# Optimization experiments

Hardware: AMD Instinct MI355X
Metric: run time of the kernel (lower is better)

Reference implementation:

```python
import jax, jax.numpy as jnp
import numpy as np

EPS = 1e-5
NEG = -1000000000.0

def _layernorm(x, g, b):
    m = x.mean(-1, keepdims=True)
    v = ((x - m) ** 2).mean(-1, keepdims=True)
    return (x - m) / jnp.sqrt(v + EPS) * g + b

D_MODEL, N_HEADS, D_K, D_V, D_FF = 768, 12, 64, 64, 3072
VOCAB, MAX_POS, N_LAYERS = 32000, 2048, 2
B, S = 2, 2048

def setup_inputs() -> dict:
    key = jax.random.key(0)
    ks = jax.random.split(key, 16)
    sc = 0.02
    L = N_LAYERS
    return {
        "inputs": jax.random.randint(ks[0], (B, S), 0, VOCAB, dtype=jnp.int64) if jax.config.jax_enable_x64 else jax.random.randint(ks[0], (B, S), 0, VOCAB, dtype=jnp.int32),
        "attention_mask": jax.random.randint(ks[1], (B, S), 0, 2, dtype=jnp.int32),
        "emb": jax.random.normal(ks[2], (VOCAB, D_MODEL), jnp.float32) * sc,
        "pos_emb": jax.random.normal(ks[3], (MAX_POS, D_MODEL), jnp.float32) * sc,
        "wq": jax.random.normal(ks[4], (L, D_MODEL, N_HEADS * D_K), jnp.float32) * sc,
        "wk": jax.random.normal(ks[5], (L, D_MODEL, N_HEADS * D_K), jnp.float32) * sc,
        "wv": jax.random.normal(ks[6], (L, D_MODEL, N_HEADS * D_V), jnp.float32) * sc,
        "wo": jax.random.normal(ks[7], (L, N_HEADS * D_V, D_MODEL), jnp.float32) * sc,
        "ln1_g": jnp.ones((L, D_MODEL), jnp.float32),
        "ln1_b": jnp.zeros((L, D_MODEL), jnp.float32),
        "w1": jax.random.normal(ks[8], (L, D_MODEL, D_FF), jnp.float32) * sc,
        "b1": jnp.zeros((L, D_FF), jnp.float32),
        "w2": jax.random.normal(ks[9], (L, D_FF, D_MODEL), jnp.float32) * sc,
        "b2": jnp.zeros((L, D_MODEL), jnp.float32),
        "ln2_g": jnp.ones((L, D_MODEL), jnp.float32),
        "ln2_b": jnp.zeros((L, D_MODEL), jnp.float32),
    }

def reference(inputs, attention_mask, emb, pos_emb, wq, wk, wv, wo,
              ln1_g, ln1_b, w1, b1, w2, b2, ln2_g, ln2_b):
    b, s = inputs.shape
    x = emb[inputs] + pos_emb[jnp.arange(s)][None, :, :]  # [B,S,D]
    # combined mask: True where pad token OR strictly-upper (future) position
    sub = jnp.triu(jnp.ones((s, s), dtype=bool), k=1)            # [S,S]
    pad = (attention_mask == 0)[:, None, :]                      # [B,1,S]
    mask = (pad | sub[None, :, :])[:, None, :, :]                # [B,1,S,S] -> broadcast over heads
    # FAITHFUL to source: masked_fill(attention_mask == 0, -1e9) fills where mask is FALSE
    scale = 1.0 / float(np.sqrt(D_K))
    attns = []
    for l in range(N_LAYERS):
        q = (x @ wq[l]).reshape(b, s, N_HEADS, D_K).transpose(0, 2, 1, 3)  # [B,H,S,dk]
        k = (x @ wk[l]).reshape(b, s, N_HEADS, D_K).transpose(0, 2, 1, 3)
        v = (x @ wv[l]).reshape(b, s, N_HEADS, D_V).transpose(0, 2, 1, 3)
        scores = jnp.einsum('bhqd,bhkd->bhqk', q, k) * scale
        scores = jnp.where(mask, scores, NEG)  # fill -1e9 where mask == False (as in source)
        attn = jax.nn.softmax(scores, axis=-1)
        ctx = jnp.einsum('bhqk,bhkd->bhqd', attn, v)
        ctx = ctx.transpose(0, 2, 1, 3).reshape(b, s, N_HEADS * D_V)
        x = _layernorm(ctx @ wo[l] + x, ln1_g[l], ln1_b[l])
        ff = jnp.maximum(x @ w1[l] + b1[l], 0.0) @ w2[l] + b2[l]
        x = _layernorm(ff + x, ln2_g[l], ln2_b[l])
        attns.append(attn)
    return x, jnp.stack(attns)  # [B,S,D], [L,B,H,S,S]
```

## Files before the change

### kernel.cpp

```cpp
#include <hip/hip_runtime.h>
#include <math.h>

#define DM 768
#define NH 12
#define DK 64
#define DFF 3072
#define BB 2
#define SS 2048
#define NL 2

typedef __attribute__((ext_vector_type(8))) short short8;
typedef __attribute__((ext_vector_type(4))) float f32x4;
typedef __attribute__((ext_vector_type(2))) unsigned int u32x2;

__device__ inline unsigned short f2bf(float f) {
    unsigned int u = __float_as_uint(f);
    u += 0x7fffu + ((u >> 16) & 1u);
    return (unsigned short)(u >> 16);
}
__device__ inline float bf2f(unsigned short h) {
    return __uint_as_float(((unsigned int)h) << 16);
}

#define GL16(g, l) __builtin_amdgcn_global_load_lds( \
    (const __attribute__((address_space(1))) void*)(g), \
    (__attribute__((address_space(3))) void*)(l), 16, 0, 0)

__global__ __launch_bounds__(256) void embed_kernel(
    const int* __restrict__ toks, const float* __restrict__ emb,
    const float* __restrict__ pos, float* __restrict__ x,
    unsigned short* __restrict__ xb)
{
    int rs = blockIdx.x;
    int s = rs & (SS - 1);
    int tok = toks[rs];
    int t = threadIdx.x;
    const float* e = emb + (size_t)tok * DM;
    const float* p = pos + (size_t)s * DM;
    float* xr = x + (size_t)rs * DM;
    unsigned short* xbr = xb + (size_t)rs * DM;
#pragma unroll
    for (int i = 0; i < 3; ++i) {
        int c = t + 256 * i;
        float v = e[c] + p[c];
        xr[c] = v;
        xbr[c] = f2bf(v);
    }
}

__global__ __launch_bounds__(256) void prep_weights(
    const float* __restrict__ wq, const float* __restrict__ wk,
    const float* __restrict__ wv, const float* __restrict__ wo,
    const float* __restrict__ w1, const float* __restrict__ w2,
    unsigned short* __restrict__ wt)
{
    __shared__ float tile[32][33];
    int id = blockIdx.x;
    int l = id / 6912; id -= l * 6912;
    unsigned short* wtl = wt + (size_t)l * 7077888;
    const float* src; unsigned short* dst; int Kd, Nd, nt, kt;
    if (id < 2304) {
        int m = id / 576, r = id % 576;
        src = ((m == 0) ? wq : (m == 1) ? wk : (m == 2) ? wv : wo) + (size_t)l * DM * DM;
        dst = wtl + (size_t)m * 589824;
        Kd = 768; Nd = 768; nt = r / 24; kt = r % 24;
    } else if (id < 4608) {
        int r = id - 2304;
        src = w1 + (size_t)l * DM * DFF; dst = wtl + 2359296; Kd = 768; Nd = 3072;
        nt = r / 24; kt = r % 24;
    } else {
        int r = id - 4608;
        src = w2 + (size_t)l * DFF * DM; dst = wtl + 4718592; Kd = 3072; Nd = 768;
        nt = r / 96; kt = r % 96;
    }
    int n0 = nt * 32, k0 = kt * 32;
    int c = threadIdx.x & 31, rr = threadIdx.x >> 5;
#pragma unroll
    for (int i = 0; i < 32; i += 8)
        tile[rr + i][c] = src[(size_t)(k0 + rr + i) * Nd + n0 + c];
    __syncthreads();
#pragma unroll
    for (int i = 0; i < 32; i += 8)
        dst[(size_t)(n0 + rr + i) * Kd + k0 + c] = f2bf(tile[c][rr + i]);
}

__global__ __launch_bounds__(256) void transpose_v(
    const unsigned short* __restrict__ vb, unsigned short* __restrict__ vt)
{
    __shared__ unsigned short tile[32][33];
    int c0 = blockIdx.x * 32;
    int r0 = blockIdx.y * 32;
    int c = threadIdx.x & 31, rr = threadIdx.x >> 5;
#pragma unroll
    for (int i = 0; i < 32; i += 8)
        tile[rr + i][c] = vb[(size_t)(r0 + rr + i) * DM + c0 + c];
    __syncthreads();
    int b = r0 >> 11;
    int s0 = r0 & 2047;
#pragma unroll
    for (int i = 0; i < 32; i += 8)
        vt[((size_t)b * DM + c0 + rr + i) * SS + s0 + c] = tile[c][rr + i];
}

template<int OUT_MODE>
__global__ __launch_bounds__(256) void gemm_bt(
    const unsigned short* __restrict__ A, const unsigned short* __restrict__ Bt,
    const float* __restrict__ bias, void* __restrict__ Cv,
    int K, int lda, int ldb, int ldc)
{
    __shared__ unsigned short As[128 * 64];
    __shared__ unsigned short Bs[128 * 64];
    const int t = threadIdx.x;
    const int row0 = blockIdx.y * 128;
    const int col0 = blockIdx.x * 128;
    const int z = (OUT_MODE == 0) ? blockIdx.z : 0;
    if (OUT_MODE == 0) { A += (size_t)z * K; Bt += (size_t)z * K; }
    const int lane = t & 63, wid = t >> 6;
    const int wr = wid >> 1, wc = wid & 1;
    const int half = lane >> 4, lr = lane & 15;
    f32x4 acc[4][4] = {};

    for (int k0 = 0; k0 < K; k0 += 64) {
#pragma unroll
        for (int r_ = 0; r_ < 4; ++r_) {
            int o_ = r_ * 4096 + t * 16;
            int row_ = o_ >> 7;
            int cp_ = (o_ >> 4) & 7;
            int gk_ = (cp_ ^ (row_ & 7)) << 3;
            GL16(A + (size_t)(row0 + row_) * lda + k0 + gk_, (char*)As + o_);
            GL16(Bt + (size_t)(col0 + row_) * ldb + k0 + gk_, (char*)Bs + o_);
        }
        __syncthreads();
#pragma unroll
        for (int kk = 0; kk < 2; ++kk) {
            short8 a_[4], b_[4];
#pragma unroll
            for (int m = 0; m < 4; ++m) {
                int row_ = wr * 64 + m * 16 + lr;
                a_[m] = *(const short8*)&As[row_ * 64 + (((kk * 4 + half) ^ (row_ & 7)) << 3)];
            }
#pragma unroll
            for (int n = 0; n < 4; ++n) {
                int row_ = wc * 64 + n * 16 + lr;
                b_[n] = *(const short8*)&Bs[row_ * 64 + (((kk * 4 + half) ^ (row_ & 7)) << 3)];
            }
#pragma unroll
            for (int m = 0; m < 4; ++m)
#pragma unroll
                for (int n = 0; n < 4; ++n)
                    acc[m][n] = __builtin_amdgcn_mfma_f32_16x16x32_bf16(a_[m], b_[n], acc[m][n], 0, 0, 0);
        }
        __syncthreads();
    }

#pragma unroll
    for (int m = 0; m < 4; ++m) {
#pragma unroll
        for (int n = 0; n < 4; ++n) {
            const int cidx = col0 + wc * 64 + n * 16 + lr;
            const float bv = bias ? bias[cidx] : 0.0f;
#pragma unroll
            for (int j = 0; j < 4; ++j) {
                const int r = row0 + wr * 64 + m * 16 + half * 4 + j;
                float v = acc[m][n][j] + bv;
                if (OUT_MODE == 2) v = fmaxf(v, 0.0f);
                if (OUT_MODE == 0) {
                    ((float*)Cv)[((size_t)z * 4096 + r) * ldc + cidx] = v;
                } else if (OUT_MODE == 4) {
                    int mi = (cidx >= 1536) ? 2 : (cidx >= 768 ? 1 : 0);
                    int cl = cidx - mi * 768;
                    ((unsigned short*)Cv)[((size_t)mi * 4096 + r) * 768 + cl] = f2bf(v);
                } else {
                    ((unsigned short*)Cv)[(size_t)r * ldc + cidx] = f2bf(v);
                }
            }
        }
    }
}

__global__ __launch_bounds__(256) void attn_fused(
    const unsigned short* __restrict__ qg, const unsigned short* __restrict__ kg,
    const unsigned short* __restrict__ vt, const int* __restrict__ amask,
    float* __restrict__ attnL, unsigned short* __restrict__ cb)
{
    __shared__ unsigned short Vs[2][64 * 128];
    __shared__ unsigned short Es[64 * 128];

    const int t = threadIdx.x;
    const int id = blockIdx.x;
    const int xcd = id & 7, idx = id >> 3;
    const int bh = xcd * 3 + (idx >> 5);
    const int qt = idx & 31;
    const int b = bh / NH, h = bh % NH;
    const int q0 = qt * 64;
    const int lane = t & 63, w = t >> 6;
    const int half = lane >> 4, lr = lane & 15;
    const int* am = amask + b * SS;

    const unsigned short* qbase = qg + ((size_t)b * SS + q0 + lr) * DM + h * DK + half * 8;
    short8 afq[4][2];
#pragma unroll
    for (int m = 0; m < 4; ++m) {
        afq[m][0] = *(const short8*)(qbase + m * 16 * DM);
        afq[m][1] = *(const short8*)(qbase + m * 16 * DM + 32);
    }

    const unsigned short* Kg = kg + (size_t)b * SS * DM + h * DK;
    const unsigned short* Vg = vt + ((size_t)b * DM + h * DK) * SS;

#define STAGE_V(kt, buf) { \
    _Pragma("unroll") \
    for (int r_ = 0; r_ < 4; ++r_) { \
        int o_ = r_ * 4096 + t * 16; \
        int d_ = o_ >> 8; \
        int cp_ = (o_ >> 4) & 15; \
        GL16(Vg + (size_t)d_ * SS + (kt) * 128 + ((cp_ ^ (d_ & 7)) << 3), (char*)Vs[buf] + o_); \
    } }

    float vsum[4] = {};
    for (int kt = 0; kt < 16; ++kt) {
#pragma unroll
        for (int nn = 0; nn < 2; ++nn) {
            const int kb = kt * 128 + w * 32 + nn * 16;
            const unsigned short* kr = Kg + (size_t)(kb + lr) * DM;
            short8 ak0 = *(const short8*)(kr + half * 8);
            short8 ak1 = *(const short8*)(kr + 32 + half * 8);
            const int pd0 = am[kb + half * 4 + 0];
            const int pd1 = am[kb + half * 4 + 1];
            const int pd2 = am[kb + half * 4 + 2];
            const int pd3 = am[kb + half * 4 + 3];
#pragma unroll
            for (int m = 0; m < 4; ++m) {
                f32x4 s = {};
                s = __builtin_amdgcn_mfma_f32_16x16x32_bf16(ak0, afq[m][0], s, 0, 0, 0);
                s = __builtin_amdgcn_mfma_f32_16x16x32_bf16(ak1, afq[m][1], s, 0, 0, 0);
                const int qpos = q0 + m * 16 + lr;
                if (pd0 == 0 || kb + half * 4 + 0 > qpos) vsum[m] += __expf(0.125f * s[0]);
                if (pd1 == 0 || kb + half * 4 + 1 > qpos) vsum[m] += __expf(0.125f * s[1]);
                if (pd2 == 0 || kb + half * 4 + 2 > qpos) vsum[m] += __expf(0.125f * s[2]);
                if (pd3 == 0 || kb + half * 4 + 3 > qpos) vsum[m] += __expf(0.125f * s[3]);
            }
        }
    }
    STAGE_V(0, 0);
    __syncthreads();

    float* red = (float*)Es;
#pragma unroll
    for (int m = 0; m < 4; ++m) {
        vsum[m] += __shfl_xor(vsum[m], 16, 64);
        vsum[m] += __shfl_xor(vsum[m], 32, 64);
    }
    if (half == 0) {
#pragma unroll
        for (int m = 0; m < 4; ++m) red[w * 64 + m * 16 + lr] = vsum[m];
    }
    __syncthreads();
    if (t < 64) {
        float rs = red[t] + red[64 + t] + red[128 + t] + red[192 + t];
        red[256 + t] = (rs > 0.0f) ? 1.0f / rs : 0.0f;
    }
    __syncthreads();
    float rinv_[4];
#pragma unroll
    for (int m = 0; m < 4; ++m) rinv_[m] = red[256 + m * 16 + lr];
    __syncthreads();

    f32x4 ctxa[4] = {};
    float* ab = attnL + ((size_t)bh * SS + q0) * SS;
    for (int kt = 0; kt < 16; ++kt) {
        if (kt == 0) {
            asm volatile("s_waitcnt vmcnt(0)" ::: "memory");
        } else {
            asm volatile("s_waitcnt vmcnt(8)" ::: "memory");
        }
        __builtin_amdgcn_s_barrier();

        short8 ak[2][2];
        int pd[2][4];
#pragma unroll
        for (int nn = 0; nn < 2; ++nn) {
            const int kb = kt * 128 + w * 32 + nn * 16;
            const unsigned short* kr = Kg + (size_t)(kb + lr) * DM;
            ak[nn][0] = *(const short8*)(kr + half * 8);
            ak[nn][1] = *(const short8*)(kr + 32 + half * 8);
#pragma unroll
            for (int j = 0; j < 4; ++j) pd[nn][j] = am[kb + half * 4 + j];
        }
        __builtin_amdgcn_sched_barrier(0);
        if (kt < 15) STAGE_V(kt + 1, (kt + 1) & 1);

#pragma unroll
        for (int nn = 0; nn < 2; ++nn) {
            const int kb = kt * 128 + w * 32 + nn * 16;
            const int colb = (w * 32 + nn * 16 + half * 4) * 2;
#pragma unroll
            for (int m = 0; m < 4; ++m) {
                f32x4 s = {};
                s = __builtin_amdgcn_mfma_f32_16x16x32_bf16(ak[nn][0], afq[m][0], s, 0, 0, 0);
                s = __builtin_amdgcn_mfma_f32_16x16x32_bf16(ak[nn][1], afq[m][1], s, 0, 0, 0);
                const int qpos = q0 + m * 16 + lr;
                float e0 = (pd[nn][0] == 0 || kb + half * 4 + 0 > qpos) ? __expf(0.125f * s[0]) * rinv_[m] : 0.0f;
                float e1 = (pd[nn][1] == 0 || kb + half * 4 + 1 > qpos) ? __expf(0.125f * s[1]) * rinv_[m] : 0.0f;
                float e2 = (pd[nn][2] == 0 || kb + half * 4 + 2 > qpos) ? __expf(0.125f * s[2]) * rinv_[m] : 0.0f;
                float e3 = (pd[nn][3] == 0 || kb + half * 4 + 3 > qpos) ? __expf(0.125f * s[3]) * rinv_[m] : 0.0f;
                u32x2 pk;
                pk[0] = ((unsigned int)f2bf(e1) << 16) | f2bf(e0);
                pk[1] = ((unsigned int)f2bf(e3) << 16) | f2bf(e2);
                const int row = m * 16 + lr;
                *(u32x2*)((char*)Es + row * 256 + (colb ^ ((lr & 7) << 4))) = pk;
            }
        }
        asm volatile("s_waitcnt lgkmcnt(0)" ::: "memory");
        __builtin_amdgcn_s_barrier();

        const char* vbuf = (const char*)Vs[kt & 1];
        __builtin_amdgcn_s_setprio(1);
#pragma unroll
        for (int ks = 0; ks < 4; ++ks) {
            const int dl = w * 16 + lr;
            const int cv = ks * 4 + half;
            short8 bv = *(const short8*)(vbuf + dl * 256 + ((cv ^ (dl & 7)) << 4));
#pragma unroll
            for (int m = 0; m < 4; ++m) {
                short8 ae = *(const short8*)((const char*)Es + (m * 16 + lr) * 256 +
                                             ((ks * 64 + half * 16) ^ ((lr & 7) << 4)));
                ctxa[m] = __builtin_amdgcn_mfma_f32_16x16x32_bf16(ae, bv, ctxa[m], 0, 0, 0);
            }
        }
        __builtin_amdgcn_s_setprio(0);

        {
            const int prow = t >> 2, pg = t & 3;
            const char* erow = (const char*)Es + prow * 256;
            const int swz = (prow & 7) << 4;
            float* drow = ab + (size_t)prow * SS + kt * 128;
#pragma unroll
            for (int c = 0; c < 4; ++c) {
                const int chunk = pg * 4 + c;
                short8 ev = *(const short8*)(erow + ((chunk * 16) ^ swz));
                float* dst = drow + chunk * 8;
                f32x4 o0, o1;
                o0[0] = bf2f((unsigned short)ev[0]); o0[1] = bf2f((unsigned short)ev[1]);
                o0[2] = bf2f((unsigned short)ev[2]); o0[3] = bf2f((unsigned short)ev[3]);
                o1[0] = bf2f((unsigned short)ev[4]); o1[1] = bf2f((unsigned short)ev[5]);
                o1[2] = bf2f((unsigned short)ev[6]); o1[3] = bf2f((unsigned short)ev[7]);
                *(f32x4*)dst = o0;
                *(f32x4*)(dst + 4) = o1;
            }
        }
    }

#pragma unroll
    for (int m = 0; m < 4; ++m)
#pragma unroll
        for (int j = 0; j < 4; ++j) {
            int row = m * 16 + half * 4 + j;
            cb[((size_t)b * SS + q0 + row) * DM + h * DK + w * 16 + lr] = f2bf(ctxa[m][j]);
        }
#undef STAGE_V
}

__global__ __launch_bounds__(256) void add_ln_kernel(
    const float* __restrict__ p0, const float* __restrict__ p1,
    const float* __restrict__ bias, const float* __restrict__ xin,
    const float* __restrict__ g, const float* __restrict__ bta,
    float* __restrict__ xout, unsigned short* __restrict__ xbout)
{
    int row = blockIdx.x;
    int t = threadIdx.x;
    const float* a0 = p0 + (size_t)row * DM;
    const float* a1 = p1 + (size_t)row * DM;
    const float* xr = xin + (size_t)row * DM;
    float* orow = xout + (size_t)row * DM;
    unsigned short* obr = xbout + (size_t)row * DM;
    __shared__ float red[256];
    float v[3];
    float sum = 0.0f;
#pragma unroll
    for (int i = 0; i < 3; ++i) {
        int c = t + 256 * i;
        v[i] = a0[c] + a1[c] + xr[c] + (bias ? bias[c] : 0.0f);
        sum += v[i];
    }
    red[t] = sum;
    __syncthreads();
    for (int s = 128; s > 0; s >>= 1) {
        if (t < s) red[t] += red[t + s];
        __syncthreads();
    }
    float mean = red[0] * (1.0f / DM);
    __syncthreads();
    float sq = 0.0f;
#pragma unroll
    for (int i = 0; i < 3; ++i) {
        float d = v[i] - mean;
        sq += d * d;
    }
    red[t] = sq;
    __syncthreads();
    for (int s = 128; s > 0; s >>= 1) {
        if (t < s) red[t] += red[t + s];
        __syncthreads();
    }
    float inv = 1.0f / sqrtf(red[0] * (1.0f / DM) + 1e-5f);
#pragma unroll
    for (int i = 0; i < 3; ++i) {
        int c = t + 256 * i;
        float ov = (v[i] - mean) * inv * g[c] + bta[c];
        orow[c] = ov;
        obr[c] = f2bf(ov);
    }
}

extern "C" void kernel_launch(void* const* d_in, const int* in_sizes, int n_in,
                              void* d_out, int out_size, void* d_ws, size_t ws_size,
                              hipStream_t stream)
{
    const int*   toks  = (const int*)d_in[0];
    const int*   amask = (const int*)d_in[1];
    const float* emb   = (const float*)d_in[2];
    const float* pos   = (const float*)d_in[3];
    const float* wq    = (const float*)d_in[4];
    const float* wk    = (const float*)d_in[5];
    const float* wv    = (const float*)d_in[6];
    const float* wo    = (const float*)d_in[7];
    const float* ln1g  = (const float*)d_in[8];
    const float* ln1b  = (const float*)d_in[9];
    const float* w1    = (const float*)d_in[10];
    const float* b1    = (const float*)d_in[11];
    const float* w2    = (const float*)d_in[12];
    const float* b2    = (const float*)d_in[13];
    const float* ln2g  = (const float*)d_in[14];
    const float* ln2b  = (const float*)d_in[15];

    float* out = (float*)d_out;
    char*  wsb = (char*)d_ws;

    const size_t ROWS = (size_t)BB * SS;
    const size_t XSZ  = ROWS * DM;
    const size_t ATTN_L = (size_t)BB * NH * SS * SS;

    float*          x    = (float*)(wsb);
    unsigned short* xb   = (unsigned short*)(wsb + 12582912);
    unsigned short* qb   = (unsigned short*)(wsb + 18874368);
    unsigned short* kbuf = (unsigned short*)(wsb + 25165824);
    unsigned short* vb   = (unsigned short*)(wsb + 31457280);
    unsigned short* cb   = (unsigned short*)(wsb + 37748736);
    float*          p0   = (float*)(wsb + 44040192);
    unsigned short* vt   = (unsigned short*)(wsb + 69206016);
    unsigned short* ffb  = (unsigned short*)(wsb + 69206016);
    unsigned short* wt   = (unsigned short*)(wsb + 94371840);

    float* attn_out = out + XSZ;

    embed_kernel<<<ROWS, 256, 0, stream>>>(toks, emb, pos, x, xb);
    prep_weights<<<13824, 256, 0, stream>>>(wq, wk, wv, wo, w1, w2, wt);

    for (int l = 0; l < NL; ++l) {
        unsigned short* QKVT = wt + (size_t)l * 7077888;
        unsigned short* WOT  = QKVT + 1769472;
        unsigned short* W1T  = QKVT + 2359296;
        unsigned short* W2T  = QKVT + 4718592;

        gemm_bt<4><<<dim3(18, 32), 256, 0, stream>>>(xb, QKVT, nullptr, qb, DM, DM, DM, DM);
        transpose_v<<<dim3(24, 128), 256, 0, stream>>>(vb, vt);

        float* attnL = attn_out + (size_t)l * ATTN_L;
        attn_fused<<<768, 256, 0, stream>>>(qb, kbuf, vt, amask, attnL, cb);

        gemm_bt<0><<<dim3(6, 32, 2), 256, 0, stream>>>(cb, WOT, nullptr, p0, 384, DM, DM, DM);
        add_ln_kernel<<<ROWS, 256, 0, stream>>>(p0, p0 + XSZ, nullptr, x,
                                                ln1g + l * DM, ln1b + l * DM, x, xb);

        gemm_bt<2><<<dim3(24, 32), 256, 0, stream>>>(xb, W1T, b1 + (size_t)l * DFF, ffb, DM, DM, DM, DFF);
        gemm_bt<0><<<dim3(6, 32, 2), 256, 0, stream>>>(ffb, W2T, nullptr, p0, 1536, DFF, DFF, DM);

        float* xdst = (l == NL - 1) ? out : x;
        add_ln_kernel<<<ROWS, 256, 0, stream>>>(p0, p0 + XSZ, b2 + (size_t)l * DM, x,
                                                ln2g + l * DM, ln2b + l * DM, xdst, xb);
    }
}
```

Before: 715.5 us.

## Pack padding mask into LDS bitmask and prefetch next K tile into registers

The padding mask is packed once per block into a 64-word LDS bitmask, which replaces repeated per-element global int loads in both the row-sum pass and the output pass. In the second pass, the K fragments for the next tile are loaded into registers alongside the V staging for the next tile, so the current tile's MFMA work overlaps those global loads. The explicit vmcnt waits are removed and the first loop gets unroll 2. Without the manual vmcnt waits, correctness of the V buffer reads now depends on the compiler inserting the right waits for the direct-to-LDS loads. That could also force waits on the prefetched K loads and reduce the overlap.

After: 711.1 us. Within noise of the previous version (-0.6%).

```diff
diff --git a/kernel.cpp b/kernel.cpp
--- a/kernel.cpp
+++ b/kernel.cpp
@@ -185,6 +185,7 @@
 {
     __shared__ unsigned short Vs[2][64 * 128];
     __shared__ unsigned short Es[64 * 128];
+    __shared__ unsigned int mbits[64];
 
     const int t = threadIdx.x;
     const int id = blockIdx.x;
@@ -197,6 +198,14 @@
     const int half = lane >> 4, lr = lane & 15;
     const int* am = amask + b * SS;
 
+    if (t < 64) {
+        unsigned int m_ = 0;
+#pragma unroll
+        for (int i = 0; i < 32; ++i)
+            m_ |= (unsigned int)(am[t * 32 + i] == 0) << i;
+        mbits[t] = m_;
+    }
+
     const unsigned short* qbase = qg + ((size_t)b * SS + q0 + lr) * DM + h * DK + half * 8;
     short8 afq[4][2];
 #pragma unroll
@@ -217,32 +226,41 @@
         GL16(Vg + (size_t)d_ * SS + (kt) * 128 + ((cp_ ^ (d_ & 7)) << 3), (char*)Vs[buf] + o_); \
     } }
 
+    __syncthreads();
+
     float vsum[4] = {};
+#pragma unroll 2
     for (int kt = 0; kt < 16; ++kt) {
 #pragma unroll
         for (int nn = 0; nn < 2; ++nn) {
             const int kb = kt * 128 + w * 32 + nn * 16;
+            const unsigned int mw = mbits[kb >> 5];
+            const int bit0 = (kb & 31) + half * 4;
             const unsigned short* kr = Kg + (size_t)(kb + lr) * DM;
             short8 ak0 = *(const short8*)(kr + half * 8);
             short8 ak1 = *(const short8*)(kr + 32 + half * 8);
-            const int pd0 = am[kb + half * 4 + 0];
-            const int pd1 = am[kb + half * 4 + 1];
-            const int pd2 = am[kb + half * 4 + 2];
-            const int pd3 = am[kb + half * 4 + 3];
 #pragma unroll
             for (int m = 0; m < 4; ++m) {
                 f32x4 s = {};
                 s = __builtin_amdgcn_mfma_f32_16x16x32_bf16(ak0, afq[m][0], s, 0, 0, 0);
                 s = __builtin_amdgcn_mfma_f32_16x16x32_bf16(ak1, afq[m][1], s, 0, 0, 0);
                 const int qpos = q0 + m * 16 + lr;
-                if (pd0 == 0 || kb + half * 4 + 0 > qpos) vsum[m] += __expf(0.125f * s[0]);
-                if (pd1 == 0 || kb + half * 4 + 1 > qpos) vsum[m] += __expf(0.125f * s[1]);
-                if (pd2 == 0 || kb + half * 4 + 2 > qpos) vsum[m] += __expf(0.125f * s[2]);
-                if (pd3 == 0 || kb + half * 4 + 3 > qpos) vsum[m] += __expf(0.125f * s[3]);
+#pragma unroll
+                for (int j = 0; j < 4; ++j) {
+                    bool keep = ((mw >> (bit0 + j)) & 1u) || (kb + half * 4 + j > qpos);
+                    vsum[m] += keep ? __expf(0.125f * s[j]) : 0.0f;
+                }
             }
         }
     }
     STAGE_V(0, 0);
+    short8 ak[2][2], akn[2][2];
+#pragma unroll
+    for (int nn = 0; nn < 2; ++nn) {
+        const unsigned short* kr = Kg + (size_t)(w * 32 + nn * 16 + lr) * DM;
+        ak[nn][0] = *(const short8*)(kr + half * 8);
+        ak[nn][1] = *(const short8*)(kr + 32 + half * 8);
+    }
     __syncthreads();
 
     float* red = (float*)Es;
@@ -269,30 +287,14 @@
     f32x4 ctxa[4] = {};
     float* ab = attnL + ((size_t)bh * SS + q0) * SS;
     for (int kt = 0; kt < 16; ++kt) {
-        if (kt == 0) {
-            asm volatile("s_waitcnt vmcnt(0)" ::: "memory");
-        } else {
-            asm volatile("s_waitcnt vmcnt(8)" ::: "memory");
-        }
+        asm volatile("" ::: "memory");
         __builtin_amdgcn_s_barrier();
 
-        short8 ak[2][2];
-        int pd[2][4];
 #pragma unroll
         for (int nn = 0; nn < 2; ++nn) {
             const int kb = kt * 128 + w * 32 + nn * 16;
-            const unsigned short* kr = Kg + (size_t)(kb + lr) * DM;
-            ak[nn][0] = *(const short8*)(kr + half * 8);
-            ak[nn][1] = *(const short8*)(kr + 32 + half * 8);
-#pragma unroll
-            for (int j = 0; j < 4; ++j) pd[nn][j] = am[kb + half * 4 + j];
-        }
-        __builtin_amdgcn_sched_barrier(0);
-        if (kt < 15) STAGE_V(kt + 1, (kt + 1) & 1);
-
-#pragma unroll
-        for (int nn = 0; nn < 2; ++nn) {
-            const int kb = kt * 128 + w * 32 + nn * 16;
+            const unsigned int mw = mbits[kb >> 5];
+            const int bit0 = (kb & 31) + half * 4;
             const int colb = (w * 32 + nn * 16 + half * 4) * 2;
 #pragma unroll
             for (int m = 0; m < 4; ++m) {
@@ -300,16 +302,25 @@
                 s = __builtin_amdgcn_mfma_f32_16x16x32_bf16(ak[nn][0], afq[m][0], s, 0, 0, 0);
                 s = __builtin_amdgcn_mfma_f32_16x16x32_bf16(ak[nn][1], afq[m][1], s, 0, 0, 0);
                 const int qpos = q0 + m * 16 + lr;
-                float e0 = (pd[nn][0] == 0 || kb + half * 4 + 0 > qpos) ? __expf(0.125f * s[0]) * rinv_[m] : 0.0f;
-                float e1 = (pd[nn][1] == 0 || kb + half * 4 + 1 > qpos) ? __expf(0.125f * s[1]) * rinv_[m] : 0.0f;
-                float e2 = (pd[nn][2] == 0 || kb + half * 4 + 2 > qpos) ? __expf(0.125f * s[2]) * rinv_[m] : 0.0f;
-                float e3 = (pd[nn][3] == 0 || kb + half * 4 + 3 > qpos) ? __expf(0.125f * s[3]) * rinv_[m] : 0.0f;
+                float e0 = (((mw >> (bit0 + 0)) & 1u) || (kb + half * 4 + 0 > qpos)) ? __expf(0.125f * s[0]) * rinv_[m] : 0.0f;
+                float e1 = (((mw >> (bit0 + 1)) & 1u) || (kb + half * 4 + 1 > qpos)) ? __expf(0.125f * s[1]) * rinv_[m] : 0.0f;
+                float e2 = (((mw >> (bit0 + 2)) & 1u) || (kb + half * 4 + 2 > qpos)) ? __expf(0.125f * s[2]) * rinv_[m] : 0.0f;
+                float e3 = (((mw >> (bit0 + 3)) & 1u) || (kb + half * 4 + 3 > qpos)) ? __expf(0.125f * s[3]) * rinv_[m] : 0.0f;
                 u32x2 pk;
                 pk[0] = ((unsigned int)f2bf(e1) << 16) | f2bf(e0);
                 pk[1] = ((unsigned int)f2bf(e3) << 16) | f2bf(e2);
                 const int row = m * 16 + lr;
                 *(u32x2*)((char*)Es + row * 256 + (colb ^ ((lr & 7) << 4))) = pk;
             }
+        }
+        if (kt < 15) {
+#pragma unroll
+            for (int nn = 0; nn < 2; ++nn) {
+                const unsigned short* kr = Kg + (size_t)((kt + 1) * 128 + w * 32 + nn * 16 + lr) * DM;
+                akn[nn][0] = *(const short8*)(kr + half * 8);
+                akn[nn][1] = *(const short8*)(kr + 32 + half * 8);
+            }
+            STAGE_V(kt + 1, (kt + 1) & 1);
         }
         asm volatile("s_waitcnt lgkmcnt(0)" ::: "memory");
         __builtin_amdgcn_s_barrier();
@@ -348,6 +359,11 @@
                 *(f32x4*)dst = o0;
                 *(f32x4*)(dst + 4) = o1;
             }
+        }
+#pragma unroll
+        for (int nn = 0; nn < 2; ++nn) {
+            ak[nn][0] = akn[nn][0];
+            ak[nn][1] = akn[nn][1];
         }
     }
 
```
